# Kernel optimization log

Hardware: AMD Instinct MI355X
Metric: run time of the kernel (lower is better)

Reference implementation:

```python
import jax, jax.numpy as jnp
import numpy as np

E = 16          # n_routed_experts
D = 2048        # embedding_dim
H = 1408        # moe_inter_dim
HS = 2 * 1408   # shared expert hidden (n_shared_experts * moe_inter_dim)
TOP_K = 6
ROUTE_SCALE = 1.0


def setup_inputs() -> dict:
    key = jax.random.key(0)
    ks = jax.random.split(key, 16)
    s = 0.02
    return {
        "x": jax.random.normal(ks[0], (4, 1024, D), dtype=jnp.float32),
        "gate_w": jax.random.normal(ks[1], (E, D), dtype=jnp.float32) * s,
        "gate_b": jax.random.normal(ks[2], (E,), dtype=jnp.float32) * s,
        "w1": jax.random.normal(ks[3], (E, H, D), dtype=jnp.float32) * s,
        "b1": jax.random.normal(ks[4], (E, H), dtype=jnp.float32) * s,
        "w2": jax.random.normal(ks[5], (E, D, H), dtype=jnp.float32) * s,
        "b2": jax.random.normal(ks[6], (E, D), dtype=jnp.float32) * s,
        "w3": jax.random.normal(ks[7], (E, H, D), dtype=jnp.float32) * s,
        "b3": jax.random.normal(ks[8], (E, H), dtype=jnp.float32) * s,
        "ws1": jax.random.normal(ks[9], (HS, D), dtype=jnp.float32) * s,
        "bs1": jax.random.normal(ks[10], (HS,), dtype=jnp.float32) * s,
        "ws2": jax.random.normal(ks[11], (D, HS), dtype=jnp.float32) * s,
        "bs2": jax.random.normal(ks[12], (D,), dtype=jnp.float32) * s,
        "ws3": jax.random.normal(ks[13], (HS, D), dtype=jnp.float32) * s,
        "bs3": jax.random.normal(ks[14], (HS,), dtype=jnp.float32) * s,
    }


def reference(x, gate_w, gate_b, w1, b1, w2, b2, w3, b3, ws1, bs1, ws2, bs2, ws3, bs3):
    shape = x.shape
    xf = x.reshape(-1, shape[-1])                       # [T, D]
    # --- Gate ---
    scores = xf @ gate_w.T                              # [T, E]
    probs = jax.nn.softmax(scores.astype(jnp.float32), axis=-1)
    biased = probs + gate_b                             # bias added after softmax
    _, idx = jax.lax.top_k(biased, TOP_K)               # [T, K]
    weights = jnp.take_along_axis(probs, idx, axis=1) * ROUTE_SCALE
    weights = weights.astype(x.dtype)                   # [T, K]
    # Combine weights as dense [T, E] (sum of top-k routing weights per expert)
    onehot = jax.nn.one_hot(idx, E, dtype=weights.dtype)  # [T, K, E]
    cw = jnp.einsum('tk,tke->te', weights, onehot)        # [T, E]
    # --- Routed experts: scan over experts, accumulate weighted SwiGLU outputs ---
    def expert_step(y, params):
        W1, B1, W2, B2, W3, B3, c = params              # c: [T]
        h = jax.nn.silu(xf @ W1.T + B1) * (xf @ W3.T + B3)  # [T, H]
        out = h @ W2.T + B2                             # [T, D]
        return y + c[:, None] * out, None
    y0 = jnp.zeros_like(xf)
    y, _ = jax.lax.scan(expert_step, y0, (w1, b1, w2, b2, w3, b3, cw.T))
    # --- Shared experts (dense SwiGLU MLP) ---
    z = (jax.nn.silu(xf @ ws1.T + bs1) * (xf @ ws3.T + bs3)) @ ws2.T + bs2
    return (y + z).reshape(shape)
```

## Files before the change

kernel.cpp:

```cpp
#include <hip/hip_runtime.h>

#define NE 16
#define DD 2048
#define HH 1408
#define HSH 2816
#define TOPK 6
#define TT 4096

typedef __bf16 bf16x8 __attribute__((ext_vector_type(8)));
typedef __bf16 bf16x4 __attribute__((ext_vector_type(4)));
typedef float f32x4 __attribute__((ext_vector_type(4)));

typedef const __attribute__((address_space(1))) void gvoid_t;
typedef __attribute__((address_space(3))) void lvoid_t;

__device__ __forceinline__ void gll16(const void* g, void* l) {
  __builtin_amdgcn_global_load_lds((gvoid_t*)g, (lvoid_t*)l, 16, 0, 0);
}

__global__ void k_cvt(const float* __restrict__ s, __bf16* __restrict__ d, long n4) {
  long i = (long)blockIdx.x * blockDim.x + threadIdx.x;
  long stride = (long)gridDim.x * blockDim.x;
  for (; i < n4; i += stride) {
    float4 v = ((const float4*)s)[i];
    bf16x4 o = { (__bf16)v.x, (__bf16)v.y, (__bf16)v.z, (__bf16)v.w };
    ((bf16x4*)d)[i] = o;
  }
}

__global__ __launch_bounds__(256) void k_gate(
    const float* __restrict__ x, const float* __restrict__ gw,
    const float* __restrict__ gb, float* __restrict__ cw,
    int* __restrict__ counts, int* __restrict__ lists,
    int* __restrict__ tok_e, int* __restrict__ tok_pos) {
  int t = blockIdx.x;
  int lane = threadIdx.x & 63, wave = threadIdx.x >> 6;
  __shared__ float sc[NE];
  const float* xt = x + (size_t)t * DD;
  for (int ei = 0; ei < 4; ++ei) {
    int e = wave * 4 + ei;
    const float* ge = gw + (size_t)e * DD;
    float s = 0.f;
    for (int j = 0; j < DD / 64; ++j) s += xt[lane + 64 * j] * ge[lane + 64 * j];
    for (int o = 32; o; o >>= 1) s += __shfl_xor(s, o);
    if (lane == 0) sc[e] = s;
  }
  __syncthreads();
  if (threadIdx.x == 0) {
    float p[NE], b[NE];
    float m = -1e30f;
    for (int e = 0; e < NE; ++e) m = fmaxf(m, sc[e]);
    float sum = 0.f;
    for (int e = 0; e < NE; ++e) { p[e] = expf(sc[e] - m); sum += p[e]; }
    float inv = 1.f / sum;
    for (int e = 0; e < NE; ++e) { p[e] *= inv; b[e] = p[e] + gb[e]; }
    float out[NE];
    bool used[NE];
    for (int e = 0; e < NE; ++e) { out[e] = 0.f; used[e] = false; }
    for (int k = 0; k < TOPK; ++k) {
      int best = -1; float bv = -1e30f;
      for (int e = 0; e < NE; ++e)
        if (!used[e] && b[e] > bv) { bv = b[e]; best = e; }
      used[best] = true;
      out[best] = p[best];
      int pos = atomicAdd(&counts[best], 1);
      lists[best * TT + pos] = t;
      tok_e[t * TOPK + k] = best;
      tok_pos[t * TOPK + k] = pos;
    }
    for (int e = 0; e < NE; ++e) cw[(size_t)t * NE + e] = out[e];
  }
}

__global__ void k_offsets(const int* __restrict__ counts, int* __restrict__ offs) {
  if (threadIdx.x == 0) {
    int a = 0;
    for (int e = 0; e < NE; ++e) { offs[e] = a; a += counts[e]; }
    offs[NE] = a;
  }
}

template <bool GATHER>
__global__ __launch_bounds__(256, 2) void k_gemm1(
    const __bf16* __restrict__ xb,
    const __bf16* __restrict__ W1, const float* __restrict__ B1,
    const __bf16* __restrict__ W3, const float* __restrict__ B3,
    __bf16* __restrict__ Hout, int Hdim,
    const int* __restrict__ counts, const int* __restrict__ offs,
    const int* __restrict__ lists) {
  int e = blockIdx.z;
  int count = GATHER ? counts[e] : TT;
  int m0 = blockIdx.y * 128;
  if (m0 >= count) return;
  int n0 = blockIdx.x * 128;
  const __bf16* W1e = W1 + (size_t)e * Hdim * DD;
  const __bf16* W3e = W3 + (size_t)e * Hdim * DD;
  const float* B1e = B1 + (size_t)e * Hdim;
  const float* B3e = B3 + (size_t)e * Hdim;
  int hbase = GATHER ? offs[e] : 0;
  const int* liste = GATHER ? lists + (size_t)e * TT : nullptr;

  __shared__ __bf16 At[128 * 64];
  __shared__ __bf16 B1t[128 * 64];
  __shared__ __bf16 B3t[128 * 64];
  __shared__ int rowtok[128];

  int tid = threadIdx.x, lane = tid & 63, wave = tid >> 6;
  if (tid < 128) {
    int s = m0 + tid;
    rowtok[tid] = GATHER ? liste[s < count ? s : 0] : (m0 + tid);
  }
  __syncthreads();

  int wm = wave >> 1, wn = wave & 1;
  f32x4 acc1[4][4] = {};
  f32x4 acc3[4][4] = {};
  int lr8 = lane >> 3;
  int lc8 = (lane & 7) * 8;
  int fr = lane & 15;
  int fk = (lane >> 4) * 8;

  for (int k0 = 0; k0 < DD; k0 += 64) {
    #pragma unroll
    for (int c = 0; c < 4; ++c) {
      int br = c * 32 + wave * 8;
      int tok = rowtok[br + lr8];
      gll16(xb + (size_t)tok * DD + k0 + lc8, &At[br * 64]);
      gll16(W1e + (size_t)(n0 + br + lr8) * DD + k0 + lc8, &B1t[br * 64]);
      gll16(W3e + (size_t)(n0 + br + lr8) * DD + k0 + lc8, &B3t[br * 64]);
    }
    __syncthreads();
    #pragma unroll
    for (int kk = 0; kk < 2; ++kk) {
      bf16x8 af[4], b1f[4], b3f[4];
      #pragma unroll
      for (int m = 0; m < 4; ++m)
        af[m] = *(const bf16x8*)&At[(wm * 64 + m * 16 + fr) * 64 + kk * 32 + fk];
      #pragma unroll
      for (int n = 0; n < 4; ++n) {
        b1f[n] = *(const bf16x8*)&B1t[(wn * 64 + n * 16 + fr) * 64 + kk * 32 + fk];
        b3f[n] = *(const bf16x8*)&B3t[(wn * 64 + n * 16 + fr) * 64 + kk * 32 + fk];
      }
      #pragma unroll
      for (int m = 0; m < 4; ++m)
        #pragma unroll
        for (int n = 0; n < 4; ++n) {
          acc1[m][n] = __builtin_amdgcn_mfma_f32_16x16x32_bf16(af[m], b1f[n], acc1[m][n], 0, 0, 0);
          acc3[m][n] = __builtin_amdgcn_mfma_f32_16x16x32_bf16(af[m], b3f[n], acc3[m][n], 0, 0, 0);
        }
    }
    __syncthreads();
  }
  #pragma unroll
  for (int m = 0; m < 4; ++m)
    #pragma unroll
    for (int n = 0; n < 4; ++n)
      #pragma unroll
      for (int j = 0; j < 4; ++j) {
        int rl = wm * 64 + m * 16 + (lane >> 4) * 4 + j;
        int s = m0 + rl;
        if (s < count) {
          int col = n0 + wn * 64 + n * 16 + fr;
          float h1 = acc1[m][n][j] + B1e[col];
          float h3 = acc3[m][n][j] + B3e[col];
          float v = h1 / (1.f + expf(-h1)) * h3;
          Hout[(size_t)(hbase + s) * Hdim + col] = (__bf16)v;
        }
      }
}

template <bool GATHER>
__global__ __launch_bounds__(256, 2) void k_gemm2(
    const __bf16* __restrict__ Hsrc, int Kd,
    const __bf16* __restrict__ W2, const float* __restrict__ B2,
    float* __restrict__ out, __bf16* __restrict__ Ybuf,
    const int* __restrict__ counts, const int* __restrict__ offs) {
  int e = blockIdx.z;
  int count = GATHER ? counts[e] : TT;
  int m0 = blockIdx.y * 128;
  if (m0 >= count) return;
  int n0 = blockIdx.x * 128;
  int hbase = GATHER ? offs[e] : 0;
  const __bf16* Ae = Hsrc + (size_t)hbase * Kd;
  const __bf16* W2e = W2 + (size_t)e * DD * Kd;
  const float* B2e = B2 + (size_t)(GATHER ? e * DD : 0);

  __shared__ __bf16 At[128 * 64];
  __shared__ __bf16 Bt[128 * 64];

  int tid = threadIdx.x, lane = tid & 63, wave = tid >> 6;
  int wm = wave >> 1, wn = wave & 1;
  f32x4 acc[4][4] = {};
  int lr8 = lane >> 3;
  int lc8 = (lane & 7) * 8;
  int fr = lane & 15;
  int fk = (lane >> 4) * 8;

  for (int k0 = 0; k0 < Kd; k0 += 64) {
    #pragma unroll
    for (int c = 0; c < 4; ++c) {
      int br = c * 32 + wave * 8;
      int sr = m0 + br + lr8;
      if (sr >= count) sr = count - 1;
      gll16(Ae + (size_t)sr * Kd + k0 + lc8, &At[br * 64]);
      gll16(W2e + (size_t)(n0 + br + lr8) * Kd + k0 + lc8, &Bt[br * 64]);
    }
    __syncthreads();
    #pragma unroll
    for (int kk = 0; kk < 2; ++kk) {
      bf16x8 af[4], bf[4];
      #pragma unroll
      for (int m = 0; m < 4; ++m)
        af[m] = *(const bf16x8*)&At[(wm * 64 + m * 16 + fr) * 64 + kk * 32 + fk];
      #pragma unroll
      for (int n = 0; n < 4; ++n)
        bf[n] = *(const bf16x8*)&Bt[(wn * 64 + n * 16 + fr) * 64 + kk * 32 + fk];
      #pragma unroll
      for (int m = 0; m < 4; ++m)
        #pragma unroll
        for (int n = 0; n < 4; ++n)
          acc[m][n] = __builtin_amdgcn_mfma_f32_16x16x32_bf16(af[m], bf[n], acc[m][n], 0, 0, 0);
    }
    __syncthreads();
  }
  #pragma unroll
  for (int m = 0; m < 4; ++m)
    #pragma unroll
    for (int n = 0; n < 4; ++n)
      #pragma unroll
      for (int j = 0; j < 4; ++j) {
        int rl = wm * 64 + m * 16 + (lane >> 4) * 4 + j;
        int s = m0 + rl;
        if (s < count) {
          int d = n0 + wn * 64 + n * 16 + fr;
          float v = acc[m][n][j] + B2e[d];
          if (GATHER)
            Ybuf[(size_t)(hbase + s) * DD + d] = (__bf16)v;
          else
            out[(size_t)s * DD + d] = v;
        }
      }
}

__global__ __launch_bounds__(256) void k_combine(
    const __bf16* __restrict__ Ybuf, const float* __restrict__ cw,
    const int* __restrict__ offs, const int* __restrict__ tok_e,
    const int* __restrict__ tok_pos, float* __restrict__ out) {
  int t = blockIdx.x;
  int tid = threadIdx.x;
  __shared__ int rws[TOPK];
  __shared__ float wsh[TOPK];
  if (tid < TOPK) {
    int e = tok_e[t * TOPK + tid];
    rws[tid] = offs[e] + tok_pos[t * TOPK + tid];
    wsh[tid] = cw[(size_t)t * NE + e];
  }
  __syncthreads();
  int d0 = tid * 8;
  float a[8];
  float4 o0 = *(const float4*)&out[(size_t)t * DD + d0];
  float4 o1 = *(const float4*)&out[(size_t)t * DD + d0 + 4];
  a[0] = o0.x; a[1] = o0.y; a[2] = o0.z; a[3] = o0.w;
  a[4] = o1.x; a[5] = o1.y; a[6] = o1.z; a[7] = o1.w;
  #pragma unroll
  for (int k = 0; k < TOPK; ++k) {
    bf16x8 v = *(const bf16x8*)&Ybuf[(size_t)rws[k] * DD + d0];
    float w = wsh[k];
    #pragma unroll
    for (int j = 0; j < 8; ++j) a[j] += w * (float)v[j];
  }
  float4 r0 = { a[0], a[1], a[2], a[3] };
  float4 r1 = { a[4], a[5], a[6], a[7] };
  *(float4*)&out[(size_t)t * DD + d0] = r0;
  *(float4*)&out[(size_t)t * DD + d0 + 4] = r1;
}

extern "C" void kernel_launch(void* const* d_in, const int* in_sizes, int n_in,
                              void* d_out, int out_size, void* d_ws, size_t ws_size,
                              hipStream_t stream) {
  const float* x      = (const float*)d_in[0];
  const float* gate_w = (const float*)d_in[1];
  const float* gate_b = (const float*)d_in[2];
  const float* w1     = (const float*)d_in[3];
  const float* b1     = (const float*)d_in[4];
  const float* w2     = (const float*)d_in[5];
  const float* b2     = (const float*)d_in[6];
  const float* w3     = (const float*)d_in[7];
  const float* b3     = (const float*)d_in[8];
  const float* ws1    = (const float*)d_in[9];
  const float* bs1    = (const float*)d_in[10];
  const float* ws2    = (const float*)d_in[11];
  const float* bs2    = (const float*)d_in[12];
  const float* ws3    = (const float*)d_in[13];
  const float* bs3    = (const float*)d_in[14];
  float* outp = (float*)d_out;

  char* ws = (char*)d_ws;
  size_t off = 0;
  auto take = [&](size_t bytes) { char* p = ws + off; off += (bytes + 255) & ~(size_t)255; return p; };
  __bf16* xb   = (__bf16*)take((size_t)TT * DD * 2);
  __bf16* w1b  = (__bf16*)take((size_t)NE * HH * DD * 2);
  __bf16* w3b  = (__bf16*)take((size_t)NE * HH * DD * 2);
  __bf16* w2b  = (__bf16*)take((size_t)NE * DD * HH * 2);
  __bf16* ws1b = (__bf16*)take((size_t)HSH * DD * 2);
  __bf16* ws3b = (__bf16*)take((size_t)HSH * DD * 2);
  __bf16* ws2b = (__bf16*)take((size_t)DD * HSH * 2);
  __bf16* Hbuf = (__bf16*)take((size_t)TT * TOPK * HH * 2);
  __bf16* Sbuf = (__bf16*)take((size_t)TT * HSH * 2);
  float*  cw   = (float*)take((size_t)TT * NE * 4);
  int*    lists  = (int*)take((size_t)NE * TT * 4);
  int*    tok_e  = (int*)take((size_t)TT * TOPK * 4);
  int*    tok_pos= (int*)take((size_t)TT * TOPK * 4);
  int*    counts = (int*)take(64);
  int*    offs   = (int*)take(128);
  __bf16* Ybuf = w1b;

  hipMemsetAsync(counts, 0, NE * sizeof(int), stream);

  k_cvt<<<2048, 256, 0, stream>>>(x, xb, (long)TT * DD / 4);
  k_cvt<<<2048, 256, 0, stream>>>(w1, w1b, (long)NE * HH * DD / 4);
  k_cvt<<<2048, 256, 0, stream>>>(w3, w3b, (long)NE * HH * DD / 4);
  k_cvt<<<2048, 256, 0, stream>>>(w2, w2b, (long)NE * DD * HH / 4);
  k_cvt<<<2048, 256, 0, stream>>>(ws1, ws1b, (long)HSH * DD / 4);
  k_cvt<<<2048, 256, 0, stream>>>(ws3, ws3b, (long)HSH * DD / 4);
  k_cvt<<<2048, 256, 0, stream>>>(ws2, ws2b, (long)DD * HSH / 4);

  k_gate<<<TT, 256, 0, stream>>>(x, gate_w, gate_b, cw, counts, lists, tok_e, tok_pos);
  k_offsets<<<1, 64, 0, stream>>>(counts, offs);

  k_gemm1<true><<<dim3(HH / 128, TT / 128, NE), 256, 0, stream>>>(
      xb, w1b, b1, w3b, b3, Hbuf, HH, counts, offs, lists);
  k_gemm1<false><<<dim3(HSH / 128, TT / 128, 1), 256, 0, stream>>>(
      xb, ws1b, bs1, ws3b, bs3, Sbuf, HSH, nullptr, nullptr, nullptr);
  k_gemm2<true><<<dim3(DD / 128, TT / 128, NE), 256, 0, stream>>>(
      Hbuf, HH, w2b, b2, nullptr, Ybuf, counts, offs);
  k_gemm2<false><<<dim3(DD / 128, TT / 128, 1), 256, 0, stream>>>(
      Sbuf, HSH, ws2b, bs2, outp, nullptr, nullptr, nullptr);
  k_combine<<<TT, 256, 0, stream>>>(Ybuf, cw, offs, tok_e, tok_pos, outp);
}
```

Measured before the change: 1.519 ms.

## Use persistent per-expert grids for routed GEMMs instead of padded 3D grids

Routed-expert GEMM kernels switch from a 3D grid sized for the worst case (TT/128 M-tiles per expert, most exiting early) to a fixed 1D grid where each block takes an (expert, N-tile) pair and loops over that expert's M-tiles with stride 2. GEMM1 also narrows its N-tile to 64 and raises occupancy to 4 blocks per CU. The shared-expert kernels become separate non-templated versions with the count checks removed. The aim is to cut the launch and scheduling cost of many empty blocks and to improve wave occupancy. The trade-off is that experts with many tokens now make a few blocks serialize over M-tiles, which can cause load imbalance.

```diff
diff --git a/kernel.cpp b/kernel.cpp
--- a/kernel.cpp
+++ b/kernel.cpp
@@ -80,38 +80,118 @@
   }
 }
 
-template <bool GATHER>
-__global__ __launch_bounds__(256, 2) void k_gemm1(
+__global__ __launch_bounds__(256, 4) void k_gemm1_p(
     const __bf16* __restrict__ xb,
     const __bf16* __restrict__ W1, const float* __restrict__ B1,
     const __bf16* __restrict__ W3, const float* __restrict__ B3,
-    __bf16* __restrict__ Hout, int Hdim,
+    __bf16* __restrict__ Hout,
     const int* __restrict__ counts, const int* __restrict__ offs,
     const int* __restrict__ lists) {
-  int e = blockIdx.z;
-  int count = GATHER ? counts[e] : TT;
+  int bid = blockIdx.x;
+  int h = bid / 352;
+  int r = bid % 352;
+  int e = r / 22;
+  int n0 = (r % 22) * 64;
+  int count = counts[e];
+  int mt = (count + 127) >> 7;
+  const __bf16* W1e = W1 + (size_t)e * HH * DD;
+  const __bf16* W3e = W3 + (size_t)e * HH * DD;
+  const float* B1e = B1 + (size_t)e * HH;
+  const float* B3e = B3 + (size_t)e * HH;
+  int hbase = offs[e];
+  const int* liste = lists + (size_t)e * TT;
+
+  __shared__ __bf16 At[128 * 64];
+  __shared__ __bf16 B1t[64 * 64];
+  __shared__ __bf16 B3t[64 * 64];
+  __shared__ int rowtok[128];
+
+  int tid = threadIdx.x, lane = tid & 63, wave = tid >> 6;
+  int wm = wave >> 1, wn = wave & 1;
+  int lr8 = lane >> 3;
+  int lc8 = (lane & 7) * 8;
+  int fr = lane & 15;
+  int fk = (lane >> 4) * 8;
+
+  for (int mi = h; mi < mt; mi += 2) {
+    int m0 = mi * 128;
+    __syncthreads();
+    if (tid < 128) {
+      int s = m0 + tid;
+      rowtok[tid] = liste[s < count ? s : count - 1];
+    }
+    __syncthreads();
+
+    f32x4 acc1[4][2] = {};
+    f32x4 acc3[4][2] = {};
+
+    for (int k0 = 0; k0 < DD; k0 += 64) {
+      #pragma unroll
+      for (int c = 0; c < 4; ++c) {
+        int br = c * 32 + wave * 8;
+        int tok = rowtok[br + lr8];
+        gll16(xb + (size_t)tok * DD + k0 + lc8, &At[br * 64]);
+      }
+      #pragma unroll
+      for (int c = 0; c < 2; ++c) {
+        int br = c * 32 + wave * 8;
+        gll16(W1e + (size_t)(n0 + br + lr8) * DD + k0 + lc8, &B1t[br * 64]);
+        gll16(W3e + (size_t)(n0 + br + lr8) * DD + k0 + lc8, &B3t[br * 64]);
+      }
+      __syncthreads();
+      #pragma unroll
+      for (int kk = 0; kk < 2; ++kk) {
+        bf16x8 af[4], b1f[2], b3f[2];
+        #pragma unroll
+        for (int m = 0; m < 4; ++m)
+          af[m] = *(const bf16x8*)&At[(wm * 64 + m * 16 + fr) * 64 + kk * 32 + fk];
+        #pragma unroll
+        for (int n = 0; n < 2; ++n) {
+          b1f[n] = *(const bf16x8*)&B1t[(wn * 32 + n * 16 + fr) * 64 + kk * 32 + fk];
+          b3f[n] = *(const bf16x8*)&B3t[(wn * 32 + n * 16 + fr) * 64 + kk * 32 + fk];
+        }
+        #pragma unroll
+        for (int m = 0; m < 4; ++m)
+          #pragma unroll
+          for (int n = 0; n < 2; ++n) {
+            acc1[m][n] = __builtin_amdgcn_mfma_f32_16x16x32_bf16(af[m], b1f[n], acc1[m][n], 0, 0, 0);
+            acc3[m][n] = __builtin_amdgcn_mfma_f32_16x16x32_bf16(af[m], b3f[n], acc3[m][n], 0, 0, 0);
+          }
+      }
+      __syncthreads();
+    }
+    #pragma unroll
+    for (int m = 0; m < 4; ++m)
+      #pragma unroll
+      for (int n = 0; n < 2; ++n)
+        #pragma unroll
+        for (int j = 0; j < 4; ++j) {
+          int rl = wm * 64 + m * 16 + (lane >> 4) * 4 + j;
+          int s = m0 + rl;
+          if (s < count) {
+            int col = n0 + wn * 32 + n * 16 + fr;
+            float h1 = acc1[m][n][j] + B1e[col];
+            float h3 = acc3[m][n][j] + B3e[col];
+            float v = h1 / (1.f + expf(-h1)) * h3;
+            Hout[(size_t)(hbase + s) * HH + col] = (__bf16)v;
+          }
+        }
+  }
+}
+
+__global__ __launch_bounds__(256, 2) void k_gemm1_s(
+    const __bf16* __restrict__ xb,
+    const __bf16* __restrict__ W1, const float* __restrict__ B1,
+    const __bf16* __restrict__ W3, const float* __restrict__ B3,
+    __bf16* __restrict__ Hout, int Hdim) {
   int m0 = blockIdx.y * 128;
-  if (m0 >= count) return;
   int n0 = blockIdx.x * 128;
-  const __bf16* W1e = W1 + (size_t)e * Hdim * DD;
-  const __bf16* W3e = W3 + (size_t)e * Hdim * DD;
-  const float* B1e = B1 + (size_t)e * Hdim;
-  const float* B3e = B3 + (size_t)e * Hdim;
-  int hbase = GATHER ? offs[e] : 0;
-  const int* liste = GATHER ? lists + (size_t)e * TT : nullptr;
 
   __shared__ __bf16 At[128 * 64];
   __shared__ __bf16 B1t[128 * 64];
   __shared__ __bf16 B3t[128 * 64];
-  __shared__ int rowtok[128];
 
   int tid = threadIdx.x, lane = tid & 63, wave = tid >> 6;
-  if (tid < 128) {
-    int s = m0 + tid;
-    rowtok[tid] = GATHER ? liste[s < count ? s : 0] : (m0 + tid);
-  }
-  __syncthreads();
-
   int wm = wave >> 1, wn = wave & 1;
   f32x4 acc1[4][4] = {};
   f32x4 acc3[4][4] = {};
@@ -124,10 +204,9 @@
     #pragma unroll
     for (int c = 0; c < 4; ++c) {
       int br = c * 32 + wave * 8;
-      int tok = rowtok[br + lr8];
-      gll16(xb + (size_t)tok * DD + k0 + lc8, &At[br * 64]);
-      gll16(W1e + (size_t)(n0 + br + lr8) * DD + k0 + lc8, &B1t[br * 64]);
-      gll16(W3e + (size_t)(n0 + br + lr8) * DD + k0 + lc8, &B3t[br * 64]);
+      gll16(xb + (size_t)(m0 + br + lr8) * DD + k0 + lc8, &At[br * 64]);
+      gll16(W1 + (size_t)(n0 + br + lr8) * DD + k0 + lc8, &B1t[br * 64]);
+      gll16(W3 + (size_t)(n0 + br + lr8) * DD + k0 + lc8, &B3t[br * 64]);
     }
     __syncthreads();
     #pragma unroll
@@ -159,31 +238,96 @@
       for (int j = 0; j < 4; ++j) {
         int rl = wm * 64 + m * 16 + (lane >> 4) * 4 + j;
         int s = m0 + rl;
-        if (s < count) {
-          int col = n0 + wn * 64 + n * 16 + fr;
-          float h1 = acc1[m][n][j] + B1e[col];
-          float h3 = acc3[m][n][j] + B3e[col];
-          float v = h1 / (1.f + expf(-h1)) * h3;
-          Hout[(size_t)(hbase + s) * Hdim + col] = (__bf16)v;
+        int col = n0 + wn * 64 + n * 16 + fr;
+        float h1 = acc1[m][n][j] + B1[0 * Hdim + col];
+        float h3 = acc3[m][n][j] + B3[0 * Hdim + col];
+        float v = h1 / (1.f + expf(-h1)) * h3;
+        Hout[(size_t)s * Hdim + col] = (__bf16)v;
+      }
+}
+
+__global__ __launch_bounds__(256, 4) void k_gemm2_p(
+    const __bf16* __restrict__ Hsrc,
+    const __bf16* __restrict__ W2, const float* __restrict__ B2,
+    __bf16* __restrict__ Ybuf,
+    const int* __restrict__ counts, const int* __restrict__ offs) {
+  int bid = blockIdx.x;
+  int h = bid / 256;
+  int r = bid % 256;
+  int e = r / 16;
+  int n0 = (r % 16) * 128;
+  int count = counts[e];
+  int mt = (count + 127) >> 7;
+  int hbase = offs[e];
+  const __bf16* Ae = Hsrc + (size_t)hbase * HH;
+  const __bf16* W2e = W2 + (size_t)e * DD * HH;
+  const float* B2e = B2 + (size_t)e * DD;
+
+  __shared__ __bf16 At[128 * 64];
+  __shared__ __bf16 Bt[128 * 64];
+
+  int tid = threadIdx.x, lane = tid & 63, wave = tid >> 6;
+  int wm = wave >> 1, wn = wave & 1;
+  int lr8 = lane >> 3;
+  int lc8 = (lane & 7) * 8;
+  int fr = lane & 15;
+  int fk = (lane >> 4) * 8;
+
+  for (int mi = h; mi < mt; mi += 2) {
+    int m0 = mi * 128;
+    __syncthreads();
+    f32x4 acc[4][4] = {};
+
+    for (int k0 = 0; k0 < HH; k0 += 64) {
+      #pragma unroll
+      for (int c = 0; c < 4; ++c) {
+        int br = c * 32 + wave * 8;
+        int sr = m0 + br + lr8;
+        if (sr >= count) sr = count - 1;
+        gll16(Ae + (size_t)sr * HH + k0 + lc8, &At[br * 64]);
+        gll16(W2e + (size_t)(n0 + br + lr8) * HH + k0 + lc8, &Bt[br * 64]);
+      }
+      __syncthreads();
+      #pragma unroll
+      for (int kk = 0; kk < 2; ++kk) {
+        bf16x8 af[4], bf[4];
+        #pragma unroll
+        for (int m = 0; m < 4; ++m)
+          af[m] = *(const bf16x8*)&At[(wm * 64 + m * 16 + fr) * 64 + kk * 32 + fk];
+        #pragma unroll
+        for (int n = 0; n < 4; ++n)
+          bf[n] = *(const bf16x8*)&Bt[(wn * 64 + n * 16 + fr) * 64 + kk * 32 + fk];
+        #pragma unroll
+        for (int m = 0; m < 4; ++m)
+          #pragma unroll
+          for (int n = 0; n < 4; ++n)
+            acc[m][n] = __builtin_amdgcn_mfma_f32_16x16x32_bf16(af[m], bf[n], acc[m][n], 0, 0, 0);
+      }
+      __syncthreads();
+    }
+    #pragma unroll
+    for (int m = 0; m < 4; ++m)
+      #pragma unroll
+      for (int n = 0; n < 4; ++n)
+        #pragma unroll
+        for (int j = 0; j < 4; ++j) {
+          int rl = wm * 64 + m * 16 + (lane >> 4) * 4 + j;
+          int s = m0 + rl;
+          if (s < count) {
+            int d = n0 + wn * 64 + n * 16 + fr;
+            float v = acc[m][n][j] + B2e[d];
+            Ybuf[(size_t)(hbase + s) * DD + d] = (__bf16)v;
+          }
         }
-      }
-}
-
-template <bool GATHER>
-__global__ __launch_bounds__(256, 2) void k_gemm2(
-    const __bf16* __restrict__ Hsrc, int Kd,
+  }
+}
+
+__global__ __launch_bounds__(256, 2) void k_gemm2_s(
+    const __bf16* __restrict__ Hsrc,
     const __bf16* __restrict__ W2, const float* __restrict__ B2,
-    float* __restrict__ out, __bf16* __restrict__ Ybuf,
-    const int* __restrict__ counts, const int* __restrict__ offs) {
-  int e = blockIdx.z;
-  int count = GATHER ? counts[e] : TT;
+    float* __restrict__ out) {
   int m0 = blockIdx.y * 128;
-  if (m0 >= count) return;
   int n0 = blockIdx.x * 128;
-  int hbase = GATHER ? offs[e] : 0;
-  const __bf16* Ae = Hsrc + (size_t)hbase * Kd;
-  const __bf16* W2e = W2 + (size_t)e * DD * Kd;
-  const float* B2e = B2 + (size_t)(GATHER ? e * DD : 0);
 
   __shared__ __bf16 At[128 * 64];
   __shared__ __bf16 Bt[128 * 64];
@@ -196,14 +340,12 @@
   int fr = lane & 15;
   int fk = (lane >> 4) * 8;
 
-  for (int k0 = 0; k0 < Kd; k0 += 64) {
+  for (int k0 = 0; k0 < HSH; k0 += 64) {
     #pragma unroll
     for (int c = 0; c < 4; ++c) {
       int br = c * 32 + wave * 8;
-      int sr = m0 + br + lr8;
-      if (sr >= count) sr = count - 1;
-      gll16(Ae + (size_t)sr * Kd + k0 + lc8, &At[br * 64]);
-      gll16(W2e + (size_t)(n0 + br + lr8) * Kd + k0 + lc8, &Bt[br * 64]);
+      gll16(Hsrc + (size_t)(m0 + br + lr8) * HSH + k0 + lc8, &At[br * 64]);
+      gll16(W2 + (size_t)(n0 + br + lr8) * HSH + k0 + lc8, &Bt[br * 64]);
     }
     __syncthreads();
     #pragma unroll
@@ -231,14 +373,8 @@
       for (int j = 0; j < 4; ++j) {
         int rl = wm * 64 + m * 16 + (lane >> 4) * 4 + j;
         int s = m0 + rl;
-        if (s < count) {
-          int d = n0 + wn * 64 + n * 16 + fr;
-          float v = acc[m][n][j] + B2e[d];
-          if (GATHER)
-            Ybuf[(size_t)(hbase + s) * DD + d] = (__bf16)v;
-          else
-            out[(size_t)s * DD + d] = v;
-        }
+        int d = n0 + wn * 64 + n * 16 + fr;
+        out[(size_t)s * DD + d] = acc[m][n][j] + B2[d];
       }
 }
 
@@ -328,13 +464,13 @@
   k_gate<<<TT, 256, 0, stream>>>(x, gate_w, gate_b, cw, counts, lists, tok_e, tok_pos);
   k_offsets<<<1, 64, 0, stream>>>(counts, offs);
 
-  k_gemm1<true><<<dim3(HH / 128, TT / 128, NE), 256, 0, stream>>>(
-      xb, w1b, b1, w3b, b3, Hbuf, HH, counts, offs, lists);
-  k_gemm1<false><<<dim3(HSH / 128, TT / 128, 1), 256, 0, stream>>>(
-      xb, ws1b, bs1, ws3b, bs3, Sbuf, HSH, nullptr, nullptr, nullptr);
-  k_gemm2<true><<<dim3(DD / 128, TT / 128, NE), 256, 0, stream>>>(
-      Hbuf, HH, w2b, b2, nullptr, Ybuf, counts, offs);
-  k_gemm2<false><<<dim3(DD / 128, TT / 128, 1), 256, 0, stream>>>(
-      Sbuf, HSH, ws2b, bs2, outp, nullptr, nullptr, nullptr);
+  k_gemm1_p<<<704, 256, 0, stream>>>(
+      xb, w1b, b1, w3b, b3, Hbuf, counts, offs, lists);
+  k_gemm1_s<<<dim3(HSH / 128, TT / 128), 256, 0, stream>>>(
+      xb, ws1b, bs1, ws3b, bs3, Sbuf, HSH);
+  k_gemm2_p<<<512, 256, 0, stream>>>(
+      Hbuf, w2b, b2, Ybuf, counts, offs);
+  k_gemm2_s<<<dim3(DD / 128, TT / 128), 256, 0, stream>>>(
+      Sbuf, ws2b, bs2, outp);
   k_combine<<<TT, 256, 0, stream>>>(Ybuf, cw, offs, tok_e, tok_pos, outp);
 }
```

Measured after the change: 1.961 ms. 29.1% more time.
